# Optimization experiments

Measured on AMD Instinct MI355X. Metric: run time of the kernel, lower is better.

Reference implementation:

```python
import jax, jax.numpy as jnp
import numpy as np
import math

B, Q, CQ = 2, 2048, 512
H, D = 8, 64  # no_heads, c_hidden

def setup_inputs() -> dict:
    key = jax.random.key(0)
    ks = jax.random.split(key, 8)
    s = 0.02
    return {
        "q_x": jax.random.normal(ks[0], (B, Q, CQ), jnp.float32),
        "kv_x": jax.random.normal(ks[1], (B, Q, CQ), jnp.float32),
        "bias": jax.random.normal(ks[2], (B, 1, Q, Q), jnp.float32),
        "w_qkv": jax.random.normal(ks[3], (3 * H * D, CQ), jnp.float32) * s,
        "w_o": jax.random.normal(ks[4], (CQ, H * D), jnp.float32) * s,
        "b_o": jnp.zeros((CQ,), jnp.float32),
        "w_g": jax.random.normal(ks[5], (H * D, CQ), jnp.float32) * s,
        "b_g": jnp.zeros((H * D,), jnp.float32),
    }

def reference(q_x, kv_x, bias, w_qkv, w_o, b_o, w_g, b_g):
    # Fused QKV projection from q_x (kv_x is unused by the original module's _prep_qkv)
    qkv = jnp.einsum('bqc,ec->bqe', q_x, w_qkv)  # [B,Q,3*H*D]
    q, k, v = jnp.split(qkv, 3, axis=-1)
    q = q.reshape(B, Q, H, D) / math.sqrt(D)
    k = k.reshape(B, Q, H, D)
    v = v.reshape(B, Q, H, D)
    # scores + additive pairwise bias, softmax over keys
    scores = jnp.einsum('bqhd,bkhd->bhqk', q, k) + bias  # [B,H,Q,K]
    attn = jax.nn.softmax(scores, axis=-1)
    o = jnp.einsum('bhqk,bkhd->bqhd', attn, v)  # [B,Q,H,D]
    # sigmoid gating
    g = jax.nn.sigmoid(jnp.einsum('bqc,ec->bqe', q_x, w_g) + b_g).reshape(B, Q, H, D)
    o = o * g
    # output projection
    o = o.reshape(B, Q, H * D)
    return jnp.einsum('bqe,ce->bqc', o, w_o) + b_o
```

## Files before the change

### kernel.cpp

```cpp
#include <hip/hip_runtime.h>
#include <math.h>

#define B_  2
#define Q_  2048
#define CQ_ 512
#define H_  8
#define D_  64
#define M_  (B_*Q_)
#define L2E 1.44269504088896f

typedef __bf16 bf16;
typedef __bf16 bf16x4 __attribute__((ext_vector_type(4)));
typedef __bf16 bf16x8 __attribute__((ext_vector_type(8)));
typedef float  f32x4  __attribute__((ext_vector_type(4)));
typedef float  f32x16 __attribute__((ext_vector_type(16)));

__device__ __forceinline__ void gl_lds16(const bf16* g, bf16* l) {
    __builtin_amdgcn_global_load_lds(
        (const __attribute__((address_space(1))) unsigned int*)g,
        (__attribute__((address_space(3))) unsigned int*)l, 16, 0, 0);
}

#define S0 (4096*512)
#define S1 (1536*512)
#define S2 (512*512)
#define S3 (512*512)
__global__ __launch_bounds__(256)
void convert_kernel(const float* __restrict__ qx, const float* __restrict__ wqkv,
                    const float* __restrict__ wg, const float* __restrict__ wo,
                    bf16* __restrict__ qxb, bf16* __restrict__ wcat, bf16* __restrict__ wob)
{
    const long long t = (long long)blockIdx.x * 256 + threadIdx.x;
    const long long e = t * 8;
    const float* src; bf16* dst;
    if (e < S0)                { src = qx + e;                  dst = qxb + e; }
    else if (e < S0 + S1)      { src = wqkv + (e - S0);         dst = wcat + (e - S0); }
    else if (e < S0 + S1 + S2) { src = wg + (e - S0 - S1);      dst = wcat + S1 + (e - S0 - S1); }
    else                       { src = wo + (e - S0 - S1 - S2); dst = wob + (e - S0 - S1 - S2); }
    const float4 a = *(const float4*)(src);
    const float4 b = *(const float4*)(src + 4);
    bf16x8 v;
    v[0] = (bf16)a.x; v[1] = (bf16)a.y; v[2] = (bf16)a.z; v[3] = (bf16)a.w;
    v[4] = (bf16)b.x; v[5] = (bf16)b.y; v[6] = (bf16)b.z; v[7] = (bf16)b.w;
    *(bf16x8*)dst = v;
}

template<int BM, int BN, int EPI>
__global__ __launch_bounds__(256)
void gemm_bf16(const bf16* __restrict__ A, const bf16* __restrict__ W,
               const float* __restrict__ bvec, float* __restrict__ fout,
               bf16* __restrict__ qb, bf16* __restrict__ kb, bf16* __restrict__ vb,
               bf16* __restrict__ gb)
{
    constexpr int MI = BM / 32, NJ = BN / 32;
    __shared__ __align__(16) bf16 As[BM * 32];
    __shared__ __align__(16) bf16 Bs[BN * 32];

    const int t = threadIdx.x;
    const int w = t >> 6, lane = t & 63;
    const int l15 = lane & 15, quad = lane >> 4;
    const int wm = w & 1, wn = w >> 1;
    const int bm = blockIdx.x * BM;
    const int bn = blockIdx.y * BN;
    const bool swapped = (EPI == 1) || ((bn >> 9) != 2);

    f32x4 acc[MI][NJ] = {};

    const int rr = t >> 2;
    const int cc = (t & 3) * 8;

    for (int k0 = 0; k0 < 512; k0 += 32) {
        #pragma unroll
        for (int i = 0; i < BM / 64; ++i)
            gl_lds16(A + (size_t)(bm + i * 64 + rr) * 512 + k0 + cc,
                     As + (i * 64 + w * 16) * 32);
        #pragma unroll
        for (int i = 0; i < BN / 64; ++i)
            gl_lds16(W + (size_t)(bn + i * 64 + rr) * 512 + k0 + cc,
                     Bs + (i * 64 + w * 16) * 32);
        __asm__ volatile("s_waitcnt vmcnt(0)" ::: "memory");
        __syncthreads();

        bf16x8 af[MI], bfr[NJ];
        #pragma unroll
        for (int i = 0; i < MI; ++i)
            af[i] = *(const bf16x8*)(As + (wm * (BM / 2) + i * 16 + l15) * 32 + quad * 8);
        #pragma unroll
        for (int j = 0; j < NJ; ++j)
            bfr[j] = *(const bf16x8*)(Bs + (wn * (BN / 2) + j * 16 + l15) * 32 + quad * 8);
        if (swapped) {
            #pragma unroll
            for (int i = 0; i < MI; ++i)
                #pragma unroll
                for (int j = 0; j < NJ; ++j)
                    acc[i][j] = __builtin_amdgcn_mfma_f32_16x16x32_bf16(bfr[j], af[i], acc[i][j], 0, 0, 0);
        } else {
            #pragma unroll
            for (int i = 0; i < MI; ++i)
                #pragma unroll
                for (int j = 0; j < NJ; ++j)
                    acc[i][j] = __builtin_amdgcn_mfma_f32_16x16x32_bf16(af[i], bfr[j], acc[i][j], 0, 0, 0);
        }
        __syncthreads();
    }

    if (swapped) {
        #pragma unroll
        for (int i = 0; i < MI; ++i) {
            const int m = bm + wm * (BM / 2) + i * 16 + l15;
            const int b = m >> 11, qq = m & 2047;
            #pragma unroll
            for (int j = 0; j < NJ; ++j) {
                const int n0 = bn + wn * (BN / 2) + j * 16 + quad * 4;
                const f32x4 cv = acc[i][j];
                if constexpr (EPI == 1) {
                    float4 st;
                    st.x = cv[0] + bvec[n0 + 0];
                    st.y = cv[1] + bvec[n0 + 1];
                    st.z = cv[2] + bvec[n0 + 2];
                    st.w = cv[3] + bvec[n0 + 3];
                    *(float4*)(fout + (size_t)m * 512 + n0) = st;
                } else {
                    const int part = n0 >> 9;
                    if (part == 0) {
                        const int h = (n0 >> 6) & 7, d0 = n0 & 63;
                        bf16x4 q4;
                        #pragma unroll
                        for (int r = 0; r < 4; ++r) q4[r] = (bf16)(cv[r] * (0.125f * L2E));
                        *(bf16x4*)(qb + (size_t)(b * H_ + h) * (Q_ * D_) + (size_t)qq * 64 + d0) = q4;
                    } else if (part == 1) {
                        const int h = (n0 >> 6) & 7, d0 = n0 & 63;
                        const size_t off = (size_t)(b * H_ + h) * (Q_ * D_)
                            + (qq >> 6) * 4096 + ((qq >> 5) & 1) * 2048
                            + (d0 >> 4) * 512 + ((d0 >> 3) & 1) * 256
                            + (qq & 31) * 8 + (d0 & 7);
                        bf16x4 k4;
                        #pragma unroll
                        for (int r = 0; r < 4; ++r) k4[r] = (bf16)cv[r];
                        *(bf16x4*)(kb + off) = k4;
                    } else {
                        const int gcol = n0 & 511;
                        const float4 bv4 = *(const float4*)(bvec + gcol);
                        bf16x4 g4;
                        g4[0] = (bf16)(1.f / (1.f + __expf(-(cv[0] + bv4.x))));
                        g4[1] = (bf16)(1.f / (1.f + __expf(-(cv[1] + bv4.y))));
                        g4[2] = (bf16)(1.f / (1.f + __expf(-(cv[2] + bv4.z))));
                        g4[3] = (bf16)(1.f / (1.f + __expf(-(cv[3] + bv4.w))));
                        *(bf16x4*)(gb + (size_t)m * 512 + gcol) = g4;
                    }
                }
            }
        }
    } else {
        #pragma unroll
        for (int i = 0; i < MI; ++i) {
            const int m0 = bm + wm * (BM / 2) + i * 16 + quad * 4;
            const int b = m0 >> 11, qq0 = m0 & 2047;
            #pragma unroll
            for (int j = 0; j < NJ; ++j) {
                const int n = bn + wn * (BN / 2) + j * 16 + l15;
                const int h = (n >> 6) & 7, d = n & 63;
                const size_t off = (size_t)(b * H_ + h) * (Q_ * D_)
                    + (qq0 >> 6) * 4096 + (d >> 5) * 2048
                    + ((qq0 & 63) >> 4) * 512 + ((qq0 >> 3) & 1) * 256
                    + (d & 31) * 8 + (qq0 & 7);
                bf16x4 v4;
                #pragma unroll
                for (int r = 0; r < 4; ++r) v4[r] = (bf16)acc[i][j][r];
                *(bf16x4*)(vb + off) = v4;
            }
        }
    }
}

__global__ __launch_bounds__(256, 3)
void attn_part(const bf16* __restrict__ qb, const bf16* __restrict__ kf,
               const bf16* __restrict__ vf, const float* __restrict__ bias,
               bf16* __restrict__ po, float* __restrict__ lsum)
{
    __shared__ __align__(16) bf16 Ks[2][4096];
    __shared__ __align__(16) bf16 Vs[2][4096];
    __shared__ __align__(16) bf16 Ps[4][32 * 72];

    const int tid  = threadIdx.x;
    const int wv   = tid >> 6, lane = tid & 63;
    const int l31  = lane & 31, b5 = lane >> 5;
    const int x    = blockIdx.x;
    const int bh   = ((x & 7) << 1) | (x >> 3);
    const int b    = bh >> 3;
    const int qg   = blockIdx.y * 128 + wv * 32 + l31;
    const int ks   = blockIdx.z;
    const int nsteps = (ks < 2) ? 12 : 8;

    const bf16* qp = qb + ((size_t)bh * Q_ + qg) * D_;
    bf16x8 bq[4];
    #pragma unroll
    for (int c = 0; c < 4; ++c)
        bq[c] = *(const bf16x8*)(qp + c * 16 + b5 * 8);

    f32x16 acc[2] = {};
    float l_loc = 0.f;

    const bf16*  kfb  = kf + (size_t)bh * (Q_ * D_) + (size_t)ks * 12 * 4096;
    const bf16*  vfb  = vf + (size_t)bh * (Q_ * D_) + (size_t)ks * 12 * 4096;
    const float* brow = bias + ((size_t)b * Q_ + qg) * Q_ + ks * 768;

    f32x4 bcur[8], bnxt[8];

    #pragma unroll
    for (int p = 0; p < 2; ++p) {
        gl_lds16(kfb + (wv * 2 + p) * 512 + lane * 8, Ks[0] + (wv * 2 + p) * 512);
        gl_lds16(vfb + (wv * 2 + p) * 512 + lane * 8, Vs[0] + (wv * 2 + p) * 512);
    }
    #pragma unroll
    for (int i = 0; i < 8; ++i)
        bcur[i] = *(const f32x4*)(brow + (i >> 2) * 32 + (i & 3) * 8 + b5 * 4);
    __asm__ volatile("s_waitcnt vmcnt(0)" ::: "memory");
    __syncthreads();

    bf16* pw = Ps[wv] + l31 * 72;

    int cur = 0;
    #pragma unroll 1
    for (int t = 0; t < nsteps; ++t) {
        if (t + 1 < nsteps) {
            const size_t off = (size_t)(t + 1) * 4096;
            #pragma unroll
            for (int p = 0; p < 2; ++p) {
                gl_lds16(kfb + off + (wv * 2 + p) * 512 + lane * 8,
                         Ks[cur ^ 1] + (wv * 2 + p) * 512);
                gl_lds16(vfb + off + (wv * 2 + p) * 512 + lane * 8,
                         Vs[cur ^ 1] + (wv * 2 + p) * 512);
            }
            const int k0n = (t + 1) * 64;
            #pragma unroll
            for (int i = 0; i < 8; ++i)
                bnxt[i] = *(const f32x4*)(brow + k0n + (i >> 2) * 32 + (i & 3) * 8 + b5 * 4);
        }

        const bf16* Kc = Ks[cur];
        f32x16 sv[2] = {};
        #pragma unroll
        for (int kg = 0; kg < 2; ++kg)
            #pragma unroll
            for (int c = 0; c < 4; ++c) {
                const bf16x8 ak = *(const bf16x8*)(Kc + kg * 2048 + c * 512 + lane * 8);
                sv[kg] = __builtin_amdgcn_mfma_f32_32x32x16_bf16(ak, bq[c], sv[kg], 0, 0, 0);
            }

        float sc[2][16];
        float rsum = 0.f;
        #pragma unroll
        for (int kg = 0; kg < 2; ++kg)
            #pragma unroll
            for (int r = 0; r < 16; ++r) {
                sc[kg][r] = __builtin_amdgcn_exp2f(
                    fmaf(bcur[kg * 4 + (r >> 2)][r & 3], L2E, sv[kg][r]));
                rsum += sc[kg][r];
            }
        l_loc += rsum;

        #pragma unroll
        for (int kg = 0; kg < 2; ++kg)
            #pragma unroll
            for (int gi = 0; gi < 4; ++gi) {
                bf16x4 p4;
                p4[0] = (bf16)sc[kg][gi * 4 + 0];
                p4[1] = (bf16)sc[kg][gi * 4 + 1];
                p4[2] = (bf16)sc[kg][gi * 4 + 2];
                p4[3] = (bf16)sc[kg][gi * 4 + 3];
                *(bf16x4*)(pw + kg * 32 + gi * 8 + b5 * 4) = p4;
            }
        __asm__ volatile("s_waitcnt lgkmcnt(0)" ::: "memory");

        const bf16* Vc = Vs[cur];
        #pragma unroll
        for (int c4 = 0; c4 < 4; ++c4) {
            const bf16x8 bp = *(const bf16x8*)(pw + c4 * 16 + b5 * 8);
            #pragma unroll
            for (int dg = 0; dg < 2; ++dg) {
                const bf16x8 av = *(const bf16x8*)(Vc + dg * 2048 + c4 * 512 + lane * 8);
                acc[dg] = __builtin_amdgcn_mfma_f32_32x32x16_bf16(av, bp, acc[dg], 0, 0, 0);
            }
        }

        if (t + 1 < nsteps) {
            #pragma unroll
            for (int i = 0; i < 8; ++i) bcur[i] = bnxt[i];
        }
        __asm__ volatile("s_waitcnt vmcnt(0)" ::: "memory");
        __syncthreads();
        cur ^= 1;
    }

    const float l_run = l_loc + __shfl_xor(l_loc, 32, 64);
    const size_t pbase = ((size_t)(ks * 16 + bh) * Q_ + qg) * 64;
    #pragma unroll
    for (int dg = 0; dg < 2; ++dg)
        #pragma unroll
        for (int gi = 0; gi < 4; ++gi) {
            const int d0 = dg * 32 + gi * 8 + b5 * 4;
            bf16x4 ov;
            #pragma unroll
            for (int r = 0; r < 4; ++r)
                ov[r] = (bf16)acc[dg][gi * 4 + r];
            *(bf16x4*)(po + pbase + d0) = ov;
        }
    if (b5 == 0)
        lsum[(size_t)(ks * 16 + bh) * Q_ + qg] = l_run;
}

__global__ __launch_bounds__(256)
void merge_kernel(const bf16* __restrict__ po, const float* __restrict__ lsum,
                  const bf16* g, bf16* og)
{
    const int gid = blockIdx.x * 256 + threadIdx.x;
    const int row = gid >> 3;
    const int d8  = (gid & 7) * 8;
    const int bh  = row >> 11, qg = row & 2047;
    const int b   = bh >> 3, h = bh & 7;

    const float inv = 1.f / (lsum[row] + lsum[16 * Q_ + row] + lsum[32 * Q_ + row]);

    const bf16x8 o0 = *(const bf16x8*)(po + (size_t)row * 64 + d8);
    const bf16x8 o1 = *(const bf16x8*)(po + (size_t)16 * Q_ * 64 + (size_t)row * 64 + d8);
    const bf16x8 o2 = *(const bf16x8*)(po + (size_t)32 * Q_ * 64 + (size_t)row * 64 + d8);
    const size_t obase = ((size_t)(b * Q_ + qg)) * 512 + h * 64 + d8;
    const bf16x8 gv = *(const bf16x8*)(g + obase);
    bf16x8 ov;
    #pragma unroll
    for (int r = 0; r < 8; ++r)
        ov[r] = (bf16)(((float)o0[r] + (float)o1[r] + (float)o2[r]) * inv * (float)gv[r]);
    *(bf16x8*)(og + obase) = ov;
}

extern "C" void kernel_launch(void* const* d_in, const int* in_sizes, int n_in,
                              void* d_out, int out_size, void* d_ws, size_t ws_size,
                              hipStream_t stream)
{
    const float* q_x   = (const float*)d_in[0];
    const float* bias  = (const float*)d_in[2];
    const float* w_qkv = (const float*)d_in[3];
    const float* w_o   = (const float*)d_in[4];
    const float* b_o   = (const float*)d_in[5];
    const float* w_g   = (const float*)d_in[6];
    const float* b_g   = (const float*)d_in[7];
    float* out = (float*)d_out;

    char* ws = (char*)d_ws;
    bf16*  po   = (bf16*)(ws);
    bf16*  qxb  = (bf16*)(ws);
    bf16*  wcat = (bf16*)(ws + (4u  << 20));
    bf16*  qb   = (bf16*)(ws + (12u << 20));
    bf16*  kb   = (bf16*)(ws + (16u << 20));
    bf16*  vb   = (bf16*)(ws + (20u << 20));
    bf16*  gb   = (bf16*)(ws + (24u << 20));
    bf16*  wob  = (bf16*)(ws + (28u << 20));
    float* lsum = (float*)(ws + (28u << 20) + (1u << 19));

    convert_kernel<<<(S0 + S1 + S2 + S3) / (256 * 8), 256, 0, stream>>>(
        q_x, w_qkv, w_g, w_o, qxb, wcat, wob);
    gemm_bf16<128, 64, 0><<<dim3(32, 32), 256, 0, stream>>>(
        qxb, wcat, b_g, nullptr, qb, kb, vb, gb);
    attn_part<<<dim3(B_ * H_, Q_ / 128, 3), 256, 0, stream>>>(qb, kb, vb, bias, po, lsum);
    merge_kernel<<<(16 * Q_ * 8) / 256, 256, 0, stream>>>(po, lsum, gb, gb);
    gemm_bf16<64, 64, 1><<<dim3(64, 8), 256, 0, stream>>>(
        gb, wob, b_o, out, nullptr, nullptr, nullptr, nullptr);
}
```

Measured before the change: 189.9 us.

## Split attention keys into two equal halves and stage K/V through registers

The key-split count for the attention partial kernel drops from three uneven chunks (12/12/8 tiles) to two equal chunks of 16 tiles. The merge kernel now sums two partials instead of three. K/V prefetch changes from direct global-to-LDS loads to register loads that are written into LDS after the compute step, and the launch-bounds occupancy hint goes from 3 to 2. The aim is to balance work across blocks and cut merge traffic, at the cost of fewer blocks (512 vs 768) for parallelism and extra register pressure.

```diff
diff --git a/kernel.cpp b/kernel.cpp
--- a/kernel.cpp
+++ b/kernel.cpp
@@ -173,7 +173,7 @@
     }
 }
 
-__global__ __launch_bounds__(256, 3)
+__global__ __launch_bounds__(256, 2)
 void attn_part(const bf16* __restrict__ qb, const bf16* __restrict__ kf,
                const bf16* __restrict__ vf, const float* __restrict__ bias,
                bf16* __restrict__ po, float* __restrict__ lsum)
@@ -190,7 +190,6 @@
     const int b    = bh >> 3;
     const int qg   = blockIdx.y * 128 + wv * 32 + l31;
     const int ks   = blockIdx.z;
-    const int nsteps = (ks < 2) ? 12 : 8;
 
     const bf16* qp = qb + ((size_t)bh * Q_ + qg) * D_;
     bf16x8 bq[4];
@@ -201,36 +200,40 @@
     f32x16 acc[2] = {};
     float l_loc = 0.f;
 
-    const bf16*  kfb  = kf + (size_t)bh * (Q_ * D_) + (size_t)ks * 12 * 4096;
-    const bf16*  vfb  = vf + (size_t)bh * (Q_ * D_) + (size_t)ks * 12 * 4096;
-    const float* brow = bias + ((size_t)b * Q_ + qg) * Q_ + ks * 768;
+    const bf16*  kfb  = kf + (size_t)bh * (Q_ * D_) + (size_t)ks * 16 * 4096;
+    const bf16*  vfb  = vf + (size_t)bh * (Q_ * D_) + (size_t)ks * 16 * 4096;
+    const float* brow = bias + ((size_t)b * Q_ + qg) * Q_ + ks * 1024;
 
     f32x4 bcur[8], bnxt[8];
-
-    #pragma unroll
-    for (int p = 0; p < 2; ++p) {
-        gl_lds16(kfb + (wv * 2 + p) * 512 + lane * 8, Ks[0] + (wv * 2 + p) * 512);
-        gl_lds16(vfb + (wv * 2 + p) * 512 + lane * 8, Vs[0] + (wv * 2 + p) * 512);
+    float4 kr[2], vr[2];
+    const int so = tid * 8;
+
+    #pragma unroll
+    for (int c = 0; c < 2; ++c) {
+        kr[c] = *(const float4*)(kfb + c * 2048 + so);
+        vr[c] = *(const float4*)(vfb + c * 2048 + so);
     }
     #pragma unroll
     for (int i = 0; i < 8; ++i)
         bcur[i] = *(const f32x4*)(brow + (i >> 2) * 32 + (i & 3) * 8 + b5 * 4);
-    __asm__ volatile("s_waitcnt vmcnt(0)" ::: "memory");
+    #pragma unroll
+    for (int c = 0; c < 2; ++c) {
+        *(float4*)(Ks[0] + c * 2048 + so) = kr[c];
+        *(float4*)(Vs[0] + c * 2048 + so) = vr[c];
+    }
     __syncthreads();
 
     bf16* pw = Ps[wv] + l31 * 72;
 
     int cur = 0;
     #pragma unroll 1
-    for (int t = 0; t < nsteps; ++t) {
-        if (t + 1 < nsteps) {
+    for (int t = 0; t < 16; ++t) {
+        if (t < 15) {
             const size_t off = (size_t)(t + 1) * 4096;
             #pragma unroll
-            for (int p = 0; p < 2; ++p) {
-                gl_lds16(kfb + off + (wv * 2 + p) * 512 + lane * 8,
-                         Ks[cur ^ 1] + (wv * 2 + p) * 512);
-                gl_lds16(vfb + off + (wv * 2 + p) * 512 + lane * 8,
-                         Vs[cur ^ 1] + (wv * 2 + p) * 512);
+            for (int c = 0; c < 2; ++c) {
+                kr[c] = *(const float4*)(kfb + off + c * 2048 + so);
+                vr[c] = *(const float4*)(vfb + off + c * 2048 + so);
             }
             const int k0n = (t + 1) * 64;
             #pragma unroll
@@ -284,11 +287,15 @@
             }
         }
 
-        if (t + 1 < nsteps) {
+        if (t < 15) {
+            #pragma unroll
+            for (int c = 0; c < 2; ++c) {
+                *(float4*)(Ks[cur ^ 1] + c * 2048 + so) = kr[c];
+                *(float4*)(Vs[cur ^ 1] + c * 2048 + so) = vr[c];
+            }
             #pragma unroll
             for (int i = 0; i < 8; ++i) bcur[i] = bnxt[i];
         }
-        __asm__ volatile("s_waitcnt vmcnt(0)" ::: "memory");
         __syncthreads();
         cur ^= 1;
     }
@@ -320,17 +327,16 @@
     const int bh  = row >> 11, qg = row & 2047;
     const int b   = bh >> 3, h = bh & 7;
 
-    const float inv = 1.f / (lsum[row] + lsum[16 * Q_ + row] + lsum[32 * Q_ + row]);
+    const float inv = 1.f / (lsum[row] + lsum[16 * Q_ + row]);
 
     const bf16x8 o0 = *(const bf16x8*)(po + (size_t)row * 64 + d8);
     const bf16x8 o1 = *(const bf16x8*)(po + (size_t)16 * Q_ * 64 + (size_t)row * 64 + d8);
-    const bf16x8 o2 = *(const bf16x8*)(po + (size_t)32 * Q_ * 64 + (size_t)row * 64 + d8);
     const size_t obase = ((size_t)(b * Q_ + qg)) * 512 + h * 64 + d8;
     const bf16x8 gv = *(const bf16x8*)(g + obase);
     bf16x8 ov;
     #pragma unroll
     for (int r = 0; r < 8; ++r)
-        ov[r] = (bf16)(((float)o0[r] + (float)o1[r] + (float)o2[r]) * inv * (float)gv[r]);
+        ov[r] = (bf16)(((float)o0[r] + (float)o1[r]) * inv * (float)gv[r]);
     *(bf16x8*)(og + obase) = ov;
 }
 
@@ -362,7 +368,7 @@
         q_x, w_qkv, w_g, w_o, qxb, wcat, wob);
     gemm_bf16<128, 64, 0><<<dim3(32, 32), 256, 0, stream>>>(
         qxb, wcat, b_g, nullptr, qb, kb, vb, gb);
-    attn_part<<<dim3(B_ * H_, Q_ / 128, 3), 256, 0, stream>>>(qb, kb, vb, bias, po, lsum);
+    attn_part<<<dim3(B_ * H_, Q_ / 128, 2), 256, 0, stream>>>(qb, kb, vb, bias, po, lsum);
     merge_kernel<<<(16 * Q_ * 8) / 256, 256, 0, stream>>>(po, lsum, gb, gb);
     gemm_bf16<64, 64, 1><<<dim3(64, 8), 256, 0, stream>>>(
         gb, wob, b_o, out, nullptr, nullptr, nullptr, nullptr);
```

New measurement: 201.5 us. +6.1%, slower.
